# Kernel tuning notes

Hardware: AMD Instinct MI355X
Metric: run time of the kernel (lower is better)

Reference implementation:

```python
import jax, jax.numpy as jnp
import numpy as np

EMBED, HEADS, LEVELS, POINTS, FFN = 256, 8, 4, 4, 1024
HD = EMBED // HEADS


def layer_norm(x, g, b, eps=1e-5):
    m = jnp.mean(x, axis=-1, keepdims=True)
    v = jnp.mean((x - m) ** 2, axis=-1, keepdims=True)
    return (x - m) / jnp.sqrt(v + eps) * g + b


def ms_deform_attn_core(value, shapes_np, loc, attn):
    # value: (B, nk, H, hd); loc: (B, nq, H, L, P, 2) normalized [0,1]; attn: (B, nq, H, L, P)
    B, nq = loc.shape[0], loc.shape[1]
    splits = np.cumsum(shapes_np[:, 0] * shapes_np[:, 1])[:-1]
    vals = jnp.split(value, splits, axis=1)
    out = jnp.zeros((B, HEADS, nq, HD), value.dtype)
    for l in range(LEVELS):
        Hl, Wl = int(shapes_np[l, 0]), int(shapes_np[l, 1])
        v = vals[l].transpose(0, 2, 1, 3)                     # (B, H, Hl*Wl, hd)
        x = loc[:, :, :, l, :, 0] * Wl - 0.5                  # (B, nq, H, P) pixel coords
        y = loc[:, :, :, l, :, 1] * Hl - 0.5
        x0 = jnp.floor(x); y0 = jnp.floor(y)
        fx = x - x0; fy = y - y0
        x0i = x0.astype(jnp.int32); y0i = y0.astype(jnp.int32)
        acc = jnp.zeros((B, HEADS, nq * POINTS, HD), value.dtype)
        for dx, dy, w in ((0, 0, (1 - fx) * (1 - fy)), (1, 0, fx * (1 - fy)),
                          (0, 1, (1 - fx) * fy), (1, 1, fx * fy)):
            xi = x0i + dx; yi = y0i + dy
            valid = (xi >= 0) & (xi < Wl) & (yi >= 0) & (yi < Hl)
            idx = jnp.clip(yi, 0, Hl - 1) * Wl + jnp.clip(xi, 0, Wl - 1)  # (B, nq, H, P)
            idx_f = idx.transpose(0, 2, 1, 3).reshape(B, HEADS, -1)
            g = jnp.take_along_axis(v, idx_f[..., None], axis=2)          # (B, H, nq*P, hd)
            wv = jnp.where(valid, w, 0.0).transpose(0, 2, 1, 3).reshape(B, HEADS, -1, 1)
            acc = acc + g * wv
        aw = attn[:, :, :, l].transpose(0, 2, 1, 3).reshape(B, HEADS, -1, 1)
        out = out + (acc * aw).reshape(B, HEADS, nq, POINTS, HD).sum(3)
    return out.transpose(0, 2, 1, 3).reshape(B, nq, EMBED)


def setup_inputs() -> dict:
    key = jax.random.key(0)
    ks = jax.random.split(key, 20)
    B = 2
    shapes = np.array([[136, 136], [68, 68], [34, 34], [17, 17]], np.int32)
    nk = int((shapes[:, 0] * shapes[:, 1]).sum())  # 24565
    lsi = np.concatenate([[0], np.cumsum(shapes[:, 0] * shapes[:, 1])[:-1]]).astype(np.int32)

    def lin(k, i, o):
        return jax.random.normal(k, (i, o), jnp.float32) * 0.02

    return {
        "src": jax.random.normal(ks[0], (B, nk, EMBED), jnp.float32),
        "reference_points": jax.random.uniform(ks[1], (B, nk, LEVELS, 2), jnp.float32),
        "spatial_shapes": jnp.asarray(shapes),
        "level_start_index": jnp.asarray(lsi),
        "w_off": lin(ks[2], EMBED, HEADS * LEVELS * POINTS * 2),
        "b_off": jax.random.normal(ks[3], (HEADS * LEVELS * POINTS * 2,), jnp.float32) * 0.5,
        "w_att": lin(ks[4], EMBED, HEADS * LEVELS * POINTS),
        "b_att": jnp.zeros((HEADS * LEVELS * POINTS,), jnp.float32),
        "w_val": lin(ks[5], EMBED, EMBED), "b_val": jnp.zeros((EMBED,), jnp.float32),
        "w_out": lin(ks[6], EMBED, EMBED), "b_out": jnp.zeros((EMBED,), jnp.float32),
        "g1": jnp.ones((EMBED,), jnp.float32), "bt1": jnp.zeros((EMBED,), jnp.float32),
        "w1": lin(ks[7], EMBED, FFN), "b1": jnp.zeros((FFN,), jnp.float32),
        "w2": lin(ks[8], FFN, EMBED), "b2": jnp.zeros((EMBED,), jnp.float32),
        "g2": jnp.ones((EMBED,), jnp.float32), "bt2": jnp.zeros((EMBED,), jnp.float32),
    }


def reference(src, reference_points, spatial_shapes, level_start_index,
              w_off, b_off, w_att, b_att, w_val, b_val, w_out, b_out,
              g1, bt1, w1, b1, w2, b2, g2, bt2):
    B, nq, D = src.shape
    shapes_np = np.asarray(spatial_shapes)
    # projections
    value = (src @ w_val + b_val).reshape(B, nq, HEADS, HD)
    off = (src @ w_off + b_off).reshape(B, nq, HEADS, LEVELS, POINTS, 2)
    attn = (src @ w_att + b_att).reshape(B, nq, HEADS, LEVELS * POINTS)
    attn = jax.nn.softmax(attn, axis=-1).reshape(B, nq, HEADS, LEVELS, POINTS)
    # sampling locations: ref + offset / [W, H] per level
    normalizer = jnp.asarray(shapes_np[:, ::-1].copy(), src.dtype)  # (L, 2) = [W, H]
    loc = reference_points[:, :, None, :, None, :] + off / normalizer[None, None, None, :, None, :]
    attn_out = ms_deform_attn_core(value, shapes_np, loc, attn) @ w_out + b_out
    x = layer_norm(src + attn_out, g1, bt1)
    ffn = jax.nn.relu(x @ w1 + b1) @ w2 + b2
    return layer_norm(x + ffn, g2, bt2)
```

## Files before the change

### kernel.cpp

```cpp
#include <hip/hip_runtime.h>
#include <math.h>

#define EMBED 256
#define HEADS 8
#define LEVELS 4
#define POINTS 4
#define FFNDIM 1024

typedef float f32x4 __attribute__((ext_vector_type(4)));
typedef float f32x2 __attribute__((ext_vector_type(2)));
typedef __bf16 bf16x8 __attribute__((ext_vector_type(8)));

static __device__ __forceinline__ float4 ld4f(const float* p) {
    return *reinterpret_cast<const float4*>(p);
}
static __device__ __forceinline__ unsigned short f2bf(float f) {
    unsigned int u = __float_as_uint(f);
    unsigned int r = (u + 0x7fffu + ((u >> 16) & 1u)) >> 16;
    return (unsigned short)r;
}
static __device__ __forceinline__ float bf2f(unsigned short u) {
    return __uint_as_float((unsigned int)u << 16);
}
static __device__ __forceinline__ f32x2 pkfma(f32x2 a, f32x2 b, f32x2 c) {
#if __has_builtin(__builtin_elementwise_fma)
    return __builtin_elementwise_fma(a, b, c);
#else
    f32x2 r; r.x = fmaf(a.x, b.x, c.x); r.y = fmaf(a.y, b.y, c.y); return r;
#endif
}
static __device__ __forceinline__
void gl_lds16(const unsigned short* g, unsigned short* l) {
    __builtin_amdgcn_global_load_lds(
        (const __attribute__((address_space(1))) unsigned int*)g,
        (__attribute__((address_space(3))) unsigned int*)l, 16, 0, 0);
}

__global__ __launch_bounds__(256)
void k_cvt_src(const float* __restrict__ src, unsigned short* __restrict__ dst, int n)
{
    int i = (blockIdx.x * 256 + threadIdx.x) * 4;
    const int stride = gridDim.x * 1024;
    for (; i < n; i += stride) {
        float4 v = ld4f(src + i);
        ushort4 o;
        o.x = f2bf(v.x); o.y = f2bf(v.y); o.z = f2bf(v.z); o.w = f2bf(v.w);
        *reinterpret_cast<ushort4*>(dst + i) = o;
    }
}

__global__ __launch_bounds__(256)
void k_cvt_w(const float* __restrict__ wv, const float* __restrict__ wo,
             const float* __restrict__ wa, const float* __restrict__ wout,
             const float* __restrict__ w1, const float* __restrict__ w2,
             unsigned short* __restrict__ wcat, unsigned short* __restrict__ woutt,
             unsigned short* __restrict__ w1t, unsigned short* __restrict__ w2t)
{
    const int total = 163840 + 65536 + 262144 + 262144;
    for (int gid = blockIdx.x * 256 + threadIdx.x; gid < total; gid += gridDim.x * 256) {
        int local = gid;
        float f; unsigned short* dst;
        if (local < 163840) {
            int n = local >> 8, k = local & 255;
            if (n < 256)      f = wv[k * 256 + n];
            else if (n < 512) f = wo[k * 256 + (n - 256)];
            else              f = wa[k * 128 + (n - 512)];
            dst = wcat + local;
        } else if ((local -= 163840) < 65536) {
            int n = local >> 8, k = local & 255;
            f = wout[k * 256 + n];
            dst = woutt + local;
        } else if ((local -= 65536) < 262144) {
            int n = local >> 8, k = local & 255;
            f = w1[k * 1024 + n];
            dst = w1t + local;
        } else {
            local -= 262144;
            int n = local >> 10, k = local & 1023;
            f = w2[k * 256 + n];
            dst = w2t + local;
        }
        *dst = f2bf(f);
    }
}


#define GEMM_STAGE(Aptr, ASTR, Wptr, WSTR, kcexp)                              \
    {                                                                          \
        int row = (wid << 3) + (lane >> 3);                                    \
        int slot = (lane & 7) ^ (row & 7);                                     \
        gl_lds16(Aptr + (size_t)(m0 + row) * ASTR + (kcexp) * 64 + slot * 8,   \
                 a_s + (size_t)(wid << 3) * 64);                               \
    }                                                                          \
    _Pragma("unroll")                                                          \
    for (int rnd = 0; rnd < 4; ++rnd) {                                        \
        int row = (rnd << 6) + (wid << 3) + (lane >> 3);                       \
        int slot = (lane & 7) ^ (row & 7);                                     \
        gl_lds16(Wptr + (size_t)(n0 + row) * WSTR + (kcexp) * 64 + slot * 8,   \
                 w_s + (size_t)((rnd << 6) + (wid << 3)) * 64);                \
    }

#define GEMM_FRAGS_MFMA                                                        \
    {                                                                          \
        bf16x8 af[2][2], bfr[4][2];                                            \
        const int ksb = (lane >> 4);                                           \
        _Pragma("unroll")                                                      \
        for (int i = 0; i < 2; ++i) {                                          \
            int m = wm * 32 + i * 16 + cl;                                     \
            _Pragma("unroll")                                                  \
            for (int kk = 0; kk < 2; ++kk) {                                   \
                int phys = (kk * 4 + ksb) ^ (m & 7);                           \
                af[i][kk] = *reinterpret_cast<const bf16x8*>(                  \
                    a_s + m * 64 + phys * 8);                                  \
            }                                                                  \
        }                                                                      \
        _Pragma("unroll")                                                      \
        for (int j = 0; j < 4; ++j) {                                          \
            int n = wn * 64 + j * 16 + cl;                                     \
            _Pragma("unroll")                                                  \
            for (int kk = 0; kk < 2; ++kk) {                                   \
                int phys = (kk * 4 + ksb) ^ (n & 7);                           \
                bfr[j][kk] = *reinterpret_cast<const bf16x8*>(                 \
                    w_s + n * 64 + phys * 8);                                  \
            }                                                                  \
        }                                                                      \
        _Pragma("unroll")                                                      \
        for (int kk = 0; kk < 2; ++kk)                                         \
            _Pragma("unroll")                                                  \
            for (int i = 0; i < 2; ++i)                                        \
                _Pragma("unroll")                                              \
                for (int j = 0; j < 4; ++j)                                    \
                    acc[i][j] = __builtin_amdgcn_mfma_f32_16x16x32_bf16(       \
                        af[i][kk], bfr[j][kk], acc[i][j], 0, 0, 0);            \
    }

__global__ __launch_bounds__(512)
void k_proj(const unsigned short* __restrict__ A, const unsigned short* __restrict__ Wt,
            const float* __restrict__ b_val, const float* __restrict__ b_off,
            const float* __restrict__ b_att,
            unsigned short* __restrict__ value, unsigned short* __restrict__ offr,
            unsigned short* __restrict__ attw, int M, int nk)
{
    __shared__ __align__(16) unsigned short smem[20480];
    unsigned short* a_s = smem;
    unsigned short* w_s = smem + 4096;
    const int tid = threadIdx.x;
    const int m0 = blockIdx.x * 64;
    const int y = blockIdx.y;
    const int n0 = y * 256;
    const int lane = tid & 63, wid = tid >> 6;
    const int wm = wid >> 2, wn = wid & 3;
    const int cl = lane & 15, r4 = (lane >> 4) * 4;

    f32x4 acc[2][4] = {};

    for (int kc = 0; kc < 4; ++kc) {
        __syncthreads();
        GEMM_STAGE(A, 256, Wt, 256, kc)
        __syncthreads();
        GEMM_FRAGS_MFMA
    }

    if (y < 2) {
        const float* bias = (y == 0) ? b_val : b_off;
        __syncthreads();
        #pragma unroll
        for (int j = 0; j < 4; ++j) {
            int col = wn * 64 + j * 16 + cl;
            float bv = bias[col];
            #pragma unroll
            for (int i = 0; i < 2; ++i)
                #pragma unroll
                for (int r = 0; r < 4; ++r)
                    smem[(wm * 32 + i * 16 + r4 + r) * 264 + col] = f2bf(acc[i][j][r] + bv);
        }
        __syncthreads();
        if (y == 0) {
            #pragma unroll
            for (int t = 0; t < 4; ++t) {
                int idx = tid + t * 512;
                int row = idx >> 5, cu = idx & 31;
                int grow = m0 + row;
                if (grow < M) {
                    int b = grow >= nk;
                    int pix = grow - (b ? nk : 0);
                    int hh = cu >> 2, ch = (cu & 3) * 8;
                    *reinterpret_cast<uint4*>(
                        value + ((size_t)(b * 8 + hh) * nk + pix) * 32 + ch) =
                        *reinterpret_cast<const uint4*>(smem + row * 264 + cu * 8);
                }
            }
        } else {
            #pragma unroll
            for (int t = 0; t < 4; ++t) {
                int idx = tid + t * 512;
                int row = idx >> 5, cu = idx & 31;
                int grow = m0 + row;
                if (grow < M)
                    *reinterpret_cast<uint4*>(offr + (size_t)grow * 256 + cu * 8) =
                        *reinterpret_cast<const uint4*>(smem + row * 264 + cu * 8);
            }
        }
    } else {
        if (wn < 2) {
            #pragma unroll
            for (int j = 0; j < 4; ++j) {
                int a = wn * 64 + j * 16 + cl;
                float bv = b_att[a];
                #pragma unroll
                for (int i = 0; i < 2; ++i) {
                    #pragma unroll
                    for (int r = 0; r < 4; ++r) {
                        float v = acc[i][j][r] + bv;
                        float mx = v;
                        mx = fmaxf(mx, __shfl_xor(mx, 1));
                        mx = fmaxf(mx, __shfl_xor(mx, 2));
                        mx = fmaxf(mx, __shfl_xor(mx, 4));
                        mx = fmaxf(mx, __shfl_xor(mx, 8));
                        float e = __expf(v - mx);
                        float s = e;
                        s += __shfl_xor(s, 1);
                        s += __shfl_xor(s, 2);
                        s += __shfl_xor(s, 4);
                        s += __shfl_xor(s, 8);
                        acc[i][j][r] = e / s;
                    }
                }
            }
        }
        __syncthreads();
        if (wn < 2) {
            #pragma unroll
            for (int j = 0; j < 4; ++j) {
                int a = wn * 64 + j * 16 + cl;
                #pragma unroll
                for (int i = 0; i < 2; ++i)
                    #pragma unroll
                    for (int r = 0; r < 4; ++r)
                        smem[(wm * 32 + i * 16 + r4 + r) * 136 + a] = f2bf(acc[i][j][r]);
            }
        }
        __syncthreads();
        #pragma unroll
        for (int t = 0; t < 2; ++t) {
            int idx = tid + t * 512;
            int row = idx >> 4, cu = idx & 15;
            int grow = m0 + row;
            if (grow < M)
                *reinterpret_cast<uint4*>(attw + (size_t)grow * 128 + cu * 8) =
                    *reinterpret_cast<const uint4*>(smem + row * 136 + cu * 8);
        }
    }
}

__global__ __launch_bounds__(256)
void k_sample(const unsigned short* __restrict__ value,
              const unsigned short* __restrict__ offr,
              const unsigned short* __restrict__ attw,
              const float* __restrict__ ref,
              const int* __restrict__ shapes, const int* __restrict__ lsi,
              unsigned short* __restrict__ core, int M)
{
    __shared__ int2 iw_s[64][65];
    const int tid = threadIdx.x;
    const int bh = blockIdx.x & 15;
    const int grp = blockIdx.x >> 4;
    const int b = bh >> 3, h = bh & 7;
    const int nk = lsi[3] + shapes[6] * shapes[7];
    const int tok0 = grp * 64;

    #pragma unroll
    for (int rnd = 0; rnd < 4; ++rnd) {
        const int lp = tid & 15;
        const int tk = rnd * 16 + (tid >> 4);
        const int l = lp >> 2;
        const int pix0 = tok0 + tk;
        int2 out[4];
        if (pix0 < nk) {
            const int token = b * nk + pix0;
            const int Hl = shapes[l * 2], Wl = shapes[l * 2 + 1];
            const int pbase = bh * nk + lsi[l];
            const float rx = ref[(size_t)token * 8 + l * 2];
            const float ry = ref[(size_t)token * 8 + l * 2 + 1];
            const unsigned int oxy = *reinterpret_cast<const unsigned int*>(
                offr + (size_t)token * 256 + (h * 16 + lp) * 2);
            const float ox = bf2f((unsigned short)(oxy & 0xffffu));
            const float oy = bf2f((unsigned short)(oxy >> 16));
            const float aw = bf2f(attw[(size_t)token * 128 + h * 16 + lp]);
            const float x = fmaf(rx, (float)Wl, ox) - 0.5f;
            const float y = fmaf(ry, (float)Hl, oy) - 0.5f;
            const float x0f = floorf(x), y0f = floorf(y);
            const float fx = x - x0f, fy = y - y0f;
            const int x0 = (int)x0f, y0 = (int)y0f;
            #pragma unroll
            for (int t = 0; t < 4; ++t) {
                const int dx = t & 1, dy = t >> 1;
                const int xi = x0 + dx, yi = y0 + dy;
                const bool valid = (xi >= 0) & (xi < Wl) & (yi >= 0) & (yi < Hl);
                const float w = (dx ? fx : 1.f - fx) * (dy ? fy : 1.f - fy) * aw;
                const int xc = min(max(xi, 0), Wl - 1);
                const int yc = min(max(yi, 0), Hl - 1);
                out[t].x = (pbase + yc * Wl + xc) * 16;
                out[t].y = __float_as_int(valid ? w : 0.f);
            }
        } else {
            #pragma unroll
            for (int t = 0; t < 4; ++t) out[t] = make_int2(0, 0);
        }
        #pragma unroll
        for (int t = 0; t < 4; ++t)
            iw_s[lp * 4 + t][tk] = out[t];
    }
    __syncthreads();

    const int tk = tid >> 2;
    const int dp = tid & 3;
    const int pix = tok0 + tk;
    const unsigned int* vu = reinterpret_cast<const unsigned int*>(value) + dp * 4;
    f32x2 a0 = {0.f, 0.f}, a1 = {0.f, 0.f};
    f32x2 a2 = {0.f, 0.f}, a3 = {0.f, 0.f};
    #pragma unroll 16
    for (int q = 0; q < 64; ++q) {
        const int2 iw = iw_s[q][tk];
        const float w = __int_as_float(iw.y);
        const f32x2 w2 = {w, w};
        const uint4 v = *reinterpret_cast<const uint4*>(vu + (size_t)(unsigned)iw.x);
        const f32x2 v0 = {__uint_as_float(v.x << 16), __uint_as_float(v.x & 0xffff0000u)};
        const f32x2 v1 = {__uint_as_float(v.y << 16), __uint_as_float(v.y & 0xffff0000u)};
        const f32x2 v2 = {__uint_as_float(v.z << 16), __uint_as_float(v.z & 0xffff0000u)};
        const f32x2 v3 = {__uint_as_float(v.w << 16), __uint_as_float(v.w & 0xffff0000u)};
        a0 = pkfma(v0, w2, a0);
        a1 = pkfma(v1, w2, a1);
        a2 = pkfma(v2, w2, a2);
        a3 = pkfma(v3, w2, a3);
    }
    if (pix < nk) {
        uint4 o;
        o.x = (unsigned int)f2bf(a0.x) | ((unsigned int)f2bf(a0.y) << 16);
        o.y = (unsigned int)f2bf(a1.x) | ((unsigned int)f2bf(a1.y) << 16);
        o.z = (unsigned int)f2bf(a2.x) | ((unsigned int)f2bf(a2.y) << 16);
        o.w = (unsigned int)f2bf(a3.x) | ((unsigned int)f2bf(a3.y) << 16);
        *reinterpret_cast<uint4*>(
            core + (size_t)(b * nk + pix) * 256 + h * 32 + dp * 8) = o;
    }
}

__global__ __launch_bounds__(512)
void k_oproj(const unsigned short* __restrict__ A, const unsigned short* __restrict__ Wt,
             const float* __restrict__ b_out, const float* __restrict__ src,
             const float* __restrict__ g1, const float* __restrict__ bt1,
             unsigned short* __restrict__ X, int M)
{
    __shared__ __align__(16) unsigned short smem[20480];
    unsigned short* a_s = smem;
    unsigned short* w_s = smem + 4096;
    __shared__ float red[64 * 8];
    __shared__ float mr[64 * 2];
    const int tid = threadIdx.x;
    const int m0 = blockIdx.x * 64;
    const int n0 = 0;
    const int lane = tid & 63, wid = tid >> 6;
    const int wm = wid >> 2, wn = wid & 3;
    const int cl = lane & 15, r4 = (lane >> 4) * 4;

    f32x4 acc[2][4] = {};

    for (int kc = 0; kc < 4; ++kc) {
        __syncthreads();
        GEMM_STAGE(A, 256, Wt, 256, kc)
        __syncthreads();
        GEMM_FRAGS_MFMA
    }

    #pragma unroll
    for (int j = 0; j < 4; ++j) {
        int col = wn * 64 + j * 16 + cl;
        float bv = b_out[col];
        #pragma unroll
        for (int i = 0; i < 2; ++i) {
            int mb = wm * 32 + i * 16 + r4;
            #pragma unroll
            for (int r = 0; r < 4; ++r) {
                int row = m0 + mb + r;
                float sv = (row < M) ? src[(size_t)row * 256 + col] : 0.f;
                acc[i][j][r] += bv + sv;
            }
        }
    }
    #pragma unroll
    for (int i = 0; i < 2; ++i)
        #pragma unroll
        for (int r = 0; r < 4; ++r) {
            float s1 = 0.f, s2 = 0.f;
            #pragma unroll
            for (int j = 0; j < 4; ++j) { float t = acc[i][j][r]; s1 += t; s2 += t * t; }
            s1 += __shfl_xor(s1, 1); s2 += __shfl_xor(s2, 1);
            s1 += __shfl_xor(s1, 2); s2 += __shfl_xor(s2, 2);
            s1 += __shfl_xor(s1, 4); s2 += __shfl_xor(s2, 4);
            s1 += __shfl_xor(s1, 8); s2 += __shfl_xor(s2, 8);
            if (cl == 0) {
                int rr = wm * 32 + i * 16 + r4 + r;
                red[(rr * 4 + wn) * 2 + 0] = s1;
                red[(rr * 4 + wn) * 2 + 1] = s2;
            }
        }
    __syncthreads();
    if (tid < 64) {
        float s1 = red[tid * 8] + red[tid * 8 + 2] + red[tid * 8 + 4] + red[tid * 8 + 6];
        float s2 = red[tid * 8 + 1] + red[tid * 8 + 3] + red[tid * 8 + 5] + red[tid * 8 + 7];
        float mu = s1 * (1.f / 256.f);
        mr[tid * 2] = mu;
        mr[tid * 2 + 1] = rsqrtf(fmaxf(s2 * (1.f / 256.f) - mu * mu, 0.f) + 1e-5f);
    }
    __syncthreads();
    #pragma unroll
    for (int j = 0; j < 4; ++j) {
        int col = wn * 64 + j * 16 + cl;
        float gv = g1[col], bt = bt1[col];
        #pragma unroll
        for (int i = 0; i < 2; ++i)
            #pragma unroll
            for (int r = 0; r < 4; ++r) {
                int rr = wm * 32 + i * 16 + r4 + r;
                smem[rr * 264 + col] =
                    f2bf((acc[i][j][r] - mr[rr * 2]) * mr[rr * 2 + 1] * gv + bt);
            }
    }
    __syncthreads();
    #pragma unroll
    for (int t = 0; t < 4; ++t) {
        int idx = tid + t * 512;
        int row = idx >> 5, cu = idx & 31;
        int grow = m0 + row;
        if (grow < M)
            *reinterpret_cast<uint4*>(X + (size_t)grow * 256 + cu * 8) =
                *reinterpret_cast<const uint4*>(smem + row * 264 + cu * 8);
    }
}

__global__ __launch_bounds__(512)
void k_ffn1(const unsigned short* __restrict__ A, const unsigned short* __restrict__ W1t,
            const float* __restrict__ B1, unsigned short* __restrict__ h, int M)
{
    __shared__ __align__(16) unsigned short smem[20480];
    unsigned short* a_s = smem;
    unsigned short* w_s = smem + 4096;
    const int tid = threadIdx.x;
    const int m0 = blockIdx.x * 64;
    const int n0 = blockIdx.y * 256;
    const int lane = tid & 63, wid = tid >> 6;
    const int wm = wid >> 2, wn = wid & 3;
    const int cl = lane & 15, r4 = (lane >> 4) * 4;

    f32x4 acc[2][4] = {};

    for (int kc = 0; kc < 4; ++kc) {
        __syncthreads();
        GEMM_STAGE(A, 256, W1t, 256, kc)
        __syncthreads();
        GEMM_FRAGS_MFMA
    }

    __syncthreads();
    #pragma unroll
    for (int j = 0; j < 4; ++j) {
        int col = wn * 64 + j * 16 + cl;
        float bv = B1[n0 + col];
        #pragma unroll
        for (int i = 0; i < 2; ++i)
            #pragma unroll
            for (int r = 0; r < 4; ++r)
                smem[(wm * 32 + i * 16 + r4 + r) * 264 + col] =
                    f2bf(fmaxf(acc[i][j][r] + bv, 0.f));
    }
    __syncthreads();
    #pragma unroll
    for (int t = 0; t < 4; ++t) {
        int idx = tid + t * 512;
        int row = idx >> 5, cu = idx & 31;
        int grow = m0 + row;
        if (grow < M)
            *reinterpret_cast<uint4*>(h + (size_t)grow * 1024 + n0 + cu * 8) =
                *reinterpret_cast<const uint4*>(smem + row * 264 + cu * 8);
    }
}

__global__ __launch_bounds__(512)
void k_ffn2(const unsigned short* __restrict__ h, const unsigned short* __restrict__ W2t,
            const float* __restrict__ B2, const unsigned short* __restrict__ Xbf,
            const float* __restrict__ G2, const float* __restrict__ BT2,
            float* __restrict__ OUT, int M)
{
    __shared__ __align__(16) unsigned short smem[20480];
    unsigned short* a_s = smem;
    unsigned short* w_s = smem + 4096;
    __shared__ float red[64 * 8];
    __shared__ float mr[64 * 2];
    const int tid = threadIdx.x;
    const int m0 = blockIdx.x * 64;
    const int n0 = 0;
    const int lane = tid & 63, wid = tid >> 6;
    const int wm = wid >> 2, wn = wid & 3;
    const int cl = lane & 15, r4 = (lane >> 4) * 4;

    f32x4 acc[2][4] = {};

    for (int kc = 0; kc < 16; ++kc) {
        __syncthreads();
        GEMM_STAGE(h, 1024, W2t, 1024, kc)
        __syncthreads();
        GEMM_FRAGS_MFMA
    }

    #pragma unroll
    for (int j = 0; j < 4; ++j) {
        int col = wn * 64 + j * 16 + cl;
        float bv = B2[col];
        #pragma unroll
        for (int i = 0; i < 2; ++i) {
            int mb = wm * 32 + i * 16 + r4;
            #pragma unroll
            for (int r = 0; r < 4; ++r) {
                int row = m0 + mb + r;
                float xv = (row < M) ? bf2f(Xbf[(size_t)row * 256 + col]) : 0.f;
                acc[i][j][r] += bv + xv;
            }
        }
    }
    #pragma unroll
    for (int i = 0; i < 2; ++i)
        #pragma unroll
        for (int r = 0; r < 4; ++r) {
            float s1 = 0.f, s2 = 0.f;
            #pragma unroll
            for (int j = 0; j < 4; ++j) { float t = acc[i][j][r]; s1 += t; s2 += t * t; }
            s1 += __shfl_xor(s1, 1); s2 += __shfl_xor(s2, 1);
            s1 += __shfl_xor(s1, 2); s2 += __shfl_xor(s2, 2);
            s1 += __shfl_xor(s1, 4); s2 += __shfl_xor(s2, 4);
            s1 += __shfl_xor(s1, 8); s2 += __shfl_xor(s2, 8);
            if (cl == 0) {
                int rr = wm * 32 + i * 16 + r4 + r;
                red[(rr * 4 + wn) * 2 + 0] = s1;
                red[(rr * 4 + wn) * 2 + 1] = s2;
            }
        }
    __syncthreads();
    if (tid < 64) {
        float s1 = red[tid * 8] + red[tid * 8 + 2] + red[tid * 8 + 4] + red[tid * 8 + 6];
        float s2 = red[tid * 8 + 1] + red[tid * 8 + 3] + red[tid * 8 + 5] + red[tid * 8 + 7];
        float mu = s1 * (1.f / 256.f);
        mr[tid * 2] = mu;
        mr[tid * 2 + 1] = rsqrtf(fmaxf(s2 * (1.f / 256.f) - mu * mu, 0.f) + 1e-5f);
    }
    __syncthreads();
    #pragma unroll
    for (int j = 0; j < 4; ++j) {
        int col = wn * 64 + j * 16 + cl;
        float gv = G2[col], bt = BT2[col];
        #pragma unroll
        for (int i = 0; i < 2; ++i) {
            int mb = wm * 32 + i * 16 + r4;
            #pragma unroll
            for (int r = 0; r < 4; ++r) {
                int rr = mb + r, row = m0 + rr;
                if (row < M)
                    OUT[(size_t)row * 256 + col] =
                        (acc[i][j][r] - mr[rr * 2]) * mr[rr * 2 + 1] * gv + bt;
            }
        }
    }
}

extern "C" void kernel_launch(void* const* d_in, const int* in_sizes, int n_in,
                              void* d_out, int out_size, void* d_ws, size_t ws_size,
                              hipStream_t stream) {
    const float* src    = (const float*)d_in[0];
    const float* ref    = (const float*)d_in[1];
    const int*   shapes = (const int*)d_in[2];
    const int*   lsi    = (const int*)d_in[3];
    const float* b_off  = (const float*)d_in[5];
    const float* b_att  = (const float*)d_in[7];
    const float* b_val  = (const float*)d_in[9];
    const float* b_out  = (const float*)d_in[11];
    const float* g1     = (const float*)d_in[12];
    const float* bt1    = (const float*)d_in[13];
    const float* b1     = (const float*)d_in[15];
    const float* b2     = (const float*)d_in[17];
    const float* g2     = (const float*)d_in[18];
    const float* bt2    = (const float*)d_in[19];
    const float* w_off  = (const float*)d_in[4];
    const float* w_att  = (const float*)d_in[6];
    const float* w_val  = (const float*)d_in[8];
    const float* w_out  = (const float*)d_in[10];
    const float* w1     = (const float*)d_in[14];
    const float* w2     = (const float*)d_in[16];

    const int M = in_sizes[0] / EMBED;
    const int nk = M / 2;
    const size_t M256 = (size_t)M * 256;

    unsigned short* w16     = (unsigned short*)d_ws;
    unsigned short* src_bf  = w16;
    unsigned short* value_bf = src_bf + M256;
    unsigned short* offr_bf = value_bf + M256;
    unsigned short* core_bf = offr_bf + M256;
    unsigned short* x_bf    = core_bf + M256;
    unsigned short* attw_bf = x_bf + M256;
    unsigned short* wcat    = attw_bf + (size_t)M * 128;
    unsigned short* woutt   = wcat + 163840;
    unsigned short* w1t     = woutt + 65536;
    unsigned short* w2t     = w1t + 262144;
    unsigned short* h_bf    = w16;

    const int gb64 = (M + 63) / 64;
    const int ngrp = (nk + 63) / 64;

    k_cvt_src<<<4096, 256, 0, stream>>>(src, src_bf, M * 256);
    k_cvt_w<<<2944, 256, 0, stream>>>(w_val, w_off, w_att, w_out, w1, w2,
                                      wcat, woutt, w1t, w2t);
    k_proj<<<dim3(gb64, 3), 512, 0, stream>>>(src_bf, wcat, b_val, b_off, b_att,
                                              value_bf, offr_bf, attw_bf, M, nk);
    k_sample<<<ngrp * 16, 256, 0, stream>>>(value_bf, offr_bf, attw_bf, ref,
                                            shapes, lsi, core_bf, M);
    k_oproj<<<gb64, 512, 0, stream>>>(core_bf, woutt, b_out, src, g1, bt1, x_bf, M);
    k_ffn1<<<dim3(gb64, 4), 512, 0, stream>>>(x_bf, w1t, b1, h_bf, M);
    k_ffn2<<<gb64, 512, 0, stream>>>(h_bf, w2t, b2, x_bf, g2, bt2,
                                     (float*)d_out, M);
}
```

Baseline: 258.8 us.

## Keep full-K A tile resident in LDS and loop over N slabs per block

The projection, output-projection and FFN1 GEMMs now stage the whole 64x256 activation tile into LDS once, then iterate over the N slabs (value/offset/attention, or the four FFN1 column slabs) inside one block instead of launching a grid dimension per slab. This avoids re-reading the A tile from global memory for every N slab. The epilogue is split into two half-row passes so it fits in the weight buffer. In exchange, LDS per block grows to 64 KB, which can cut occupancy, and the grid shrinks by 3-4x, so the GPU is filled with fewer, longer blocks.

```diff
diff --git a/kernel.cpp b/kernel.cpp
--- a/kernel.cpp
+++ b/kernel.cpp
@@ -85,33 +85,37 @@
 }
 
 
-#define GEMM_STAGE(Aptr, ASTR, Wptr, WSTR, kcexp)                              \
-    {                                                                          \
-        int row = (wid << 3) + (lane >> 3);                                    \
-        int slot = (lane & 7) ^ (row & 7);                                     \
-        gl_lds16(Aptr + (size_t)(m0 + row) * ASTR + (kcexp) * 64 + slot * 8,   \
-                 a_s + (size_t)(wid << 3) * 64);                               \
-    }                                                                          \
+#define STAGE_A_RES(Aptr, ASTR)                                                \
     _Pragma("unroll")                                                          \
-    for (int rnd = 0; rnd < 4; ++rnd) {                                        \
+    for (int it = 0; it < 4; ++it) {                                           \
+        int g = it * 512 + wid * 64 + lane;                                    \
+        int row = g >> 5, c = g & 31;                                          \
+        int s = c ^ (row & 7);                                                 \
+        gl_lds16(Aptr + (size_t)(m0 + row) * ASTR + s * 8,                     \
+                 a_s + (size_t)(it * 512 + wid * 64) * 8);                     \
+    }
+
+#define STAGE_W_SLAB(Wptr, WSTR, NRND, kcexp)                                  \
+    _Pragma("unroll")                                                          \
+    for (int rnd = 0; rnd < NRND; ++rnd) {                                     \
         int row = (rnd << 6) + (wid << 3) + (lane >> 3);                       \
         int slot = (lane & 7) ^ (row & 7);                                     \
         gl_lds16(Wptr + (size_t)(n0 + row) * WSTR + (kcexp) * 64 + slot * 8,   \
                  w_s + (size_t)((rnd << 6) + (wid << 3)) * 64);                \
     }
 
-#define GEMM_FRAGS_MFMA                                                        \
+#define KSTEP_4J(kcv)                                                          \
     {                                                                          \
+        const int ksb = (lane >> 4);                                           \
         bf16x8 af[2][2], bfr[4][2];                                            \
-        const int ksb = (lane >> 4);                                           \
         _Pragma("unroll")                                                      \
         for (int i = 0; i < 2; ++i) {                                          \
             int m = wm * 32 + i * 16 + cl;                                     \
             _Pragma("unroll")                                                  \
             for (int kk = 0; kk < 2; ++kk) {                                   \
-                int phys = (kk * 4 + ksb) ^ (m & 7);                           \
+                int phys = (kcv) * 8 + (((kk << 2) + ksb) ^ (m & 7));          \
                 af[i][kk] = *reinterpret_cast<const bf16x8*>(                  \
-                    a_s + m * 64 + phys * 8);                                  \
+                    a_s + m * 256 + phys * 8);                                 \
             }                                                                  \
         }                                                                      \
         _Pragma("unroll")                                                      \
@@ -119,7 +123,7 @@
             int n = wn * 64 + j * 16 + cl;                                     \
             _Pragma("unroll")                                                  \
             for (int kk = 0; kk < 2; ++kk) {                                   \
-                int phys = (kk * 4 + ksb) ^ (n & 7);                           \
+                int phys = ((kk << 2) + ksb) ^ (n & 7);                        \
                 bfr[j][kk] = *reinterpret_cast<const bf16x8*>(                 \
                     w_s + n * 64 + phys * 8);                                  \
             }                                                                  \
@@ -141,104 +145,137 @@
             unsigned short* __restrict__ value, unsigned short* __restrict__ offr,
             unsigned short* __restrict__ attw, int M, int nk)
 {
-    __shared__ __align__(16) unsigned short smem[20480];
-    unsigned short* a_s = smem;
-    unsigned short* w_s = smem + 4096;
+    __shared__ __align__(16) unsigned short a_s[64 * 256];
+    __shared__ __align__(16) unsigned short w_s[256 * 64];
     const int tid = threadIdx.x;
     const int m0 = blockIdx.x * 64;
-    const int y = blockIdx.y;
-    const int n0 = y * 256;
     const int lane = tid & 63, wid = tid >> 6;
     const int wm = wid >> 2, wn = wid & 3;
     const int cl = lane & 15, r4 = (lane >> 4) * 4;
 
-    f32x4 acc[2][4] = {};
-
-    for (int kc = 0; kc < 4; ++kc) {
-        __syncthreads();
-        GEMM_STAGE(A, 256, Wt, 256, kc)
-        __syncthreads();
-        GEMM_FRAGS_MFMA
-    }
-
-    if (y < 2) {
-        const float* bias = (y == 0) ? b_val : b_off;
-        __syncthreads();
-        #pragma unroll
-        for (int j = 0; j < 4; ++j) {
-            int col = wn * 64 + j * 16 + cl;
-            float bv = bias[col];
-            #pragma unroll
-            for (int i = 0; i < 2; ++i)
-                #pragma unroll
-                for (int r = 0; r < 4; ++r)
-                    smem[(wm * 32 + i * 16 + r4 + r) * 264 + col] = f2bf(acc[i][j][r] + bv);
-        }
-        __syncthreads();
-        if (y == 0) {
-            #pragma unroll
-            for (int t = 0; t < 4; ++t) {
+    STAGE_A_RES(A, 256)
+
+    for (int sl = 0; sl < 2; ++sl) {
+        const int n0 = sl * 256;
+        f32x4 acc[2][4] = {};
+        for (int kc = 0; kc < 4; ++kc) {
+            __syncthreads();
+            STAGE_W_SLAB(Wt, 256, 4, kc)
+            __syncthreads();
+            KSTEP_4J(kc)
+        }
+        const float* bias = (sl == 0) ? b_val : b_off;
+        #pragma unroll
+        for (int hh = 0; hh < 2; ++hh) {
+            __syncthreads();
+            if (wm == hh) {
+                #pragma unroll
+                for (int j = 0; j < 4; ++j) {
+                    int col = wn * 64 + j * 16 + cl;
+                    float bv = bias[col];
+                    #pragma unroll
+                    for (int i = 0; i < 2; ++i)
+                        #pragma unroll
+                        for (int r = 0; r < 4; ++r)
+                            w_s[(i * 16 + r4 + r) * 264 + col] =
+                                f2bf(acc[i][j][r] + bv);
+                }
+            }
+            __syncthreads();
+            #pragma unroll
+            for (int t = 0; t < 2; ++t) {
                 int idx = tid + t * 512;
                 int row = idx >> 5, cu = idx & 31;
-                int grow = m0 + row;
+                int grow = m0 + hh * 32 + row;
                 if (grow < M) {
-                    int b = grow >= nk;
-                    int pix = grow - (b ? nk : 0);
-                    int hh = cu >> 2, ch = (cu & 3) * 8;
-                    *reinterpret_cast<uint4*>(
-                        value + ((size_t)(b * 8 + hh) * nk + pix) * 32 + ch) =
-                        *reinterpret_cast<const uint4*>(smem + row * 264 + cu * 8);
-                }
-            }
-        } else {
-            #pragma unroll
-            for (int t = 0; t < 4; ++t) {
-                int idx = tid + t * 512;
-                int row = idx >> 5, cu = idx & 31;
-                int grow = m0 + row;
-                if (grow < M)
-                    *reinterpret_cast<uint4*>(offr + (size_t)grow * 256 + cu * 8) =
-                        *reinterpret_cast<const uint4*>(smem + row * 264 + cu * 8);
-            }
-        }
-    } else {
-        if (wn < 2) {
-            #pragma unroll
-            for (int j = 0; j < 4; ++j) {
-                int a = wn * 64 + j * 16 + cl;
-                float bv = b_att[a];
-                #pragma unroll
-                for (int i = 0; i < 2; ++i) {
-                    #pragma unroll
-                    for (int r = 0; r < 4; ++r) {
-                        float v = acc[i][j][r] + bv;
-                        float mx = v;
-                        mx = fmaxf(mx, __shfl_xor(mx, 1));
-                        mx = fmaxf(mx, __shfl_xor(mx, 2));
-                        mx = fmaxf(mx, __shfl_xor(mx, 4));
-                        mx = fmaxf(mx, __shfl_xor(mx, 8));
-                        float e = __expf(v - mx);
-                        float s = e;
-                        s += __shfl_xor(s, 1);
-                        s += __shfl_xor(s, 2);
-                        s += __shfl_xor(s, 4);
-                        s += __shfl_xor(s, 8);
-                        acc[i][j][r] = e / s;
+                    uint4 vv = *reinterpret_cast<const uint4*>(w_s + row * 264 + cu * 8);
+                    if (sl == 0) {
+                        int b = grow >= nk;
+                        int pix = grow - (b ? nk : 0);
+                        int hd = cu >> 2, ch = (cu & 3) * 8;
+                        *reinterpret_cast<uint4*>(
+                            value + ((size_t)(b * 8 + hd) * nk + pix) * 32 + ch) = vv;
+                    } else {
+                        *reinterpret_cast<uint4*>(offr + (size_t)grow * 256 + cu * 8) = vv;
                     }
                 }
             }
         }
+    }
+
+    {
+        const int n0 = 512;
+        f32x4 acc[2][2] = {};
+        for (int kc = 0; kc < 4; ++kc) {
+            __syncthreads();
+            STAGE_W_SLAB(Wt, 256, 2, kc)
+            __syncthreads();
+            {
+                const int ksb = (lane >> 4);
+                bf16x8 af[2][2], bfr[2][2];
+                #pragma unroll
+                for (int i = 0; i < 2; ++i) {
+                    int m = wm * 32 + i * 16 + cl;
+                    #pragma unroll
+                    for (int kk = 0; kk < 2; ++kk) {
+                        int phys = kc * 8 + (((kk << 2) + ksb) ^ (m & 7));
+                        af[i][kk] = *reinterpret_cast<const bf16x8*>(
+                            a_s + m * 256 + phys * 8);
+                    }
+                }
+                #pragma unroll
+                for (int j = 0; j < 2; ++j) {
+                    int n = wn * 32 + j * 16 + cl;
+                    #pragma unroll
+                    for (int kk = 0; kk < 2; ++kk) {
+                        int phys = ((kk << 2) + ksb) ^ (n & 7);
+                        bfr[j][kk] = *reinterpret_cast<const bf16x8*>(
+                            w_s + n * 64 + phys * 8);
+                    }
+                }
+                #pragma unroll
+                for (int kk = 0; kk < 2; ++kk)
+                    #pragma unroll
+                    for (int i = 0; i < 2; ++i)
+                        #pragma unroll
+                        for (int j = 0; j < 2; ++j)
+                            acc[i][j] = __builtin_amdgcn_mfma_f32_16x16x32_bf16(
+                                af[i][kk], bfr[j][kk], acc[i][j], 0, 0, 0);
+            }
+        }
+        #pragma unroll
+        for (int j = 0; j < 2; ++j) {
+            int a = wn * 32 + j * 16 + cl;
+            float bv = b_att[a];
+            #pragma unroll
+            for (int i = 0; i < 2; ++i) {
+                #pragma unroll
+                for (int r = 0; r < 4; ++r) {
+                    float v = acc[i][j][r] + bv;
+                    float mx = v;
+                    mx = fmaxf(mx, __shfl_xor(mx, 1));
+                    mx = fmaxf(mx, __shfl_xor(mx, 2));
+                    mx = fmaxf(mx, __shfl_xor(mx, 4));
+                    mx = fmaxf(mx, __shfl_xor(mx, 8));
+                    float e = __expf(v - mx);
+                    float s = e;
+                    s += __shfl_xor(s, 1);
+                    s += __shfl_xor(s, 2);
+                    s += __shfl_xor(s, 4);
+                    s += __shfl_xor(s, 8);
+                    acc[i][j][r] = e / s;
+                }
+            }
+        }
         __syncthreads();
-        if (wn < 2) {
-            #pragma unroll
-            for (int j = 0; j < 4; ++j) {
-                int a = wn * 64 + j * 16 + cl;
-                #pragma unroll
-                for (int i = 0; i < 2; ++i)
-                    #pragma unroll
-                    for (int r = 0; r < 4; ++r)
-                        smem[(wm * 32 + i * 16 + r4 + r) * 136 + a] = f2bf(acc[i][j][r]);
-            }
+        #pragma unroll
+        for (int j = 0; j < 2; ++j) {
+            int a = wn * 32 + j * 16 + cl;
+            #pragma unroll
+            for (int i = 0; i < 2; ++i)
+                #pragma unroll
+                for (int r = 0; r < 4; ++r)
+                    w_s[(wm * 32 + i * 16 + r4 + r) * 136 + a] = f2bf(acc[i][j][r]);
         }
         __syncthreads();
         #pragma unroll
@@ -248,7 +285,7 @@
             int grow = m0 + row;
             if (grow < M)
                 *reinterpret_cast<uint4*>(attw + (size_t)grow * 128 + cu * 8) =
-                    *reinterpret_cast<const uint4*>(smem + row * 136 + cu * 8);
+                    *reinterpret_cast<const uint4*>(w_s + row * 136 + cu * 8);
         }
     }
 }
@@ -351,9 +388,8 @@
              const float* __restrict__ g1, const float* __restrict__ bt1,
              unsigned short* __restrict__ X, int M)
 {
-    __shared__ __align__(16) unsigned short smem[20480];
-    unsigned short* a_s = smem;
-    unsigned short* w_s = smem + 4096;
+    __shared__ __align__(16) unsigned short a_s[64 * 256];
+    __shared__ __align__(16) unsigned short w_s[256 * 64];
     __shared__ float red[64 * 8];
     __shared__ float mr[64 * 2];
     const int tid = threadIdx.x;
@@ -363,13 +399,14 @@
     const int wm = wid >> 2, wn = wid & 3;
     const int cl = lane & 15, r4 = (lane >> 4) * 4;
 
+    STAGE_A_RES(A, 256)
+
     f32x4 acc[2][4] = {};
-
     for (int kc = 0; kc < 4; ++kc) {
         __syncthreads();
-        GEMM_STAGE(A, 256, Wt, 256, kc)
+        STAGE_W_SLAB(Wt, 256, 4, kc)
         __syncthreads();
-        GEMM_FRAGS_MFMA
+        KSTEP_4J(kc)
     }
 
     #pragma unroll
@@ -414,27 +451,34 @@
     }
     __syncthreads();
     #pragma unroll
-    for (int j = 0; j < 4; ++j) {
-        int col = wn * 64 + j * 16 + cl;
-        float gv = g1[col], bt = bt1[col];
-        #pragma unroll
-        for (int i = 0; i < 2; ++i)
-            #pragma unroll
-            for (int r = 0; r < 4; ++r) {
-                int rr = wm * 32 + i * 16 + r4 + r;
-                smem[rr * 264 + col] =
-                    f2bf((acc[i][j][r] - mr[rr * 2]) * mr[rr * 2 + 1] * gv + bt);
-            }
-    }
-    __syncthreads();
-    #pragma unroll
-    for (int t = 0; t < 4; ++t) {
-        int idx = tid + t * 512;
-        int row = idx >> 5, cu = idx & 31;
-        int grow = m0 + row;
-        if (grow < M)
-            *reinterpret_cast<uint4*>(X + (size_t)grow * 256 + cu * 8) =
-                *reinterpret_cast<const uint4*>(smem + row * 264 + cu * 8);
+    for (int hh = 0; hh < 2; ++hh) {
+        __syncthreads();
+        if (wm == hh) {
+            #pragma unroll
+            for (int j = 0; j < 4; ++j) {
+                int col = wn * 64 + j * 16 + cl;
+                float gv = g1[col], bt = bt1[col];
+                #pragma unroll
+                for (int i = 0; i < 2; ++i)
+                    #pragma unroll
+                    for (int r = 0; r < 4; ++r) {
+                        int lr = i * 16 + r4 + r;
+                        int rr = hh * 32 + lr;
+                        w_s[lr * 264 + col] =
+                            f2bf((acc[i][j][r] - mr[rr * 2]) * mr[rr * 2 + 1] * gv + bt);
+                    }
+            }
+        }
+        __syncthreads();
+        #pragma unroll
+        for (int t = 0; t < 2; ++t) {
+            int idx = tid + t * 512;
+            int row = idx >> 5, cu = idx & 31;
+            int grow = m0 + hh * 32 + row;
+            if (grow < M)
+                *reinterpret_cast<uint4*>(X + (size_t)grow * 256 + cu * 8) =
+                    *reinterpret_cast<const uint4*>(w_s + row * 264 + cu * 8);
+        }
     }
 }
 
@@ -442,48 +486,69 @@
 void k_ffn1(const unsigned short* __restrict__ A, const unsigned short* __restrict__ W1t,
             const float* __restrict__ B1, unsigned short* __restrict__ h, int M)
 {
-    __shared__ __align__(16) unsigned short smem[20480];
-    unsigned short* a_s = smem;
-    unsigned short* w_s = smem + 4096;
+    __shared__ __align__(16) unsigned short a_s[64 * 256];
+    __shared__ __align__(16) unsigned short w_s[256 * 64];
     const int tid = threadIdx.x;
     const int m0 = blockIdx.x * 64;
-    const int n0 = blockIdx.y * 256;
     const int lane = tid & 63, wid = tid >> 6;
     const int wm = wid >> 2, wn = wid & 3;
     const int cl = lane & 15, r4 = (lane >> 4) * 4;
 
-    f32x4 acc[2][4] = {};
-
-    for (int kc = 0; kc < 4; ++kc) {
-        __syncthreads();
-        GEMM_STAGE(A, 256, W1t, 256, kc)
-        __syncthreads();
-        GEMM_FRAGS_MFMA
-    }
-
-    __syncthreads();
-    #pragma unroll
-    for (int j = 0; j < 4; ++j) {
-        int col = wn * 64 + j * 16 + cl;
-        float bv = B1[n0 + col];
-        #pragma unroll
-        for (int i = 0; i < 2; ++i)
-            #pragma unroll
-            for (int r = 0; r < 4; ++r)
-                smem[(wm * 32 + i * 16 + r4 + r) * 264 + col] =
-                    f2bf(fmaxf(acc[i][j][r] + bv, 0.f));
-    }
-    __syncthreads();
-    #pragma unroll
-    for (int t = 0; t < 4; ++t) {
-        int idx = tid + t * 512;
-        int row = idx >> 5, cu = idx & 31;
-        int grow = m0 + row;
-        if (grow < M)
-            *reinterpret_cast<uint4*>(h + (size_t)grow * 1024 + n0 + cu * 8) =
-                *reinterpret_cast<const uint4*>(smem + row * 264 + cu * 8);
-    }
-}
+    STAGE_A_RES(A, 256)
+
+    for (int sl = 0; sl < 4; ++sl) {
+        const int n0 = sl * 256;
+        f32x4 acc[2][4] = {};
+        for (int kc = 0; kc < 4; ++kc) {
+            __syncthreads();
+            STAGE_W_SLAB(W1t, 256, 4, kc)
+            __syncthreads();
+            KSTEP_4J(kc)
+        }
+        #pragma unroll
+        for (int hh = 0; hh < 2; ++hh) {
+            __syncthreads();
+            if (wm == hh) {
+                #pragma unroll
+                for (int j = 0; j < 4; ++j) {
+                    int col = wn * 64 + j * 16 + cl;
+                    float bv = B1[n0 + col];
+                    #pragma unroll
+                    for (int i = 0; i < 2; ++i)
+                        #pragma unroll
+                        for (int r = 0; r < 4; ++r)
+                            w_s[(i * 16 + r4 + r) * 264 + col] =
+                                f2bf(fmaxf(acc[i][j][r] + bv, 0.f));
+                }
+            }
+            __syncthreads();
+            #pragma unroll
+            for (int t = 0; t < 2; ++t) {
+                int idx = tid + t * 512;
+                int row = idx >> 5, cu = idx & 31;
+                int grow = m0 + hh * 32 + row;
+                if (grow < M)
+                    *reinterpret_cast<uint4*>(h + (size_t)grow * 1024 + n0 + cu * 8) =
+                        *reinterpret_cast<const uint4*>(w_s + row * 264 + cu * 8);
+            }
+        }
+    }
+}
+
+#define GEMM_STAGE2(Aptr, ASTR, Wptr, WSTR, kcexp)                             \
+    {                                                                          \
+        int row = (wid << 3) + (lane >> 3);                                    \
+        int slot = (lane & 7) ^ (row & 7);                                     \
+        gl_lds16(Aptr + (size_t)(m0 + row) * ASTR + (kcexp) * 64 + slot * 8,   \
+                 a2_s + (size_t)(wid << 3) * 64);                              \
+    }                                                                          \
+    _Pragma("unroll")                                                          \
+    for (int rnd = 0; rnd < 4; ++rnd) {                                        \
+        int row = (rnd << 6) + (wid << 3) + (lane >> 3);                       \
+        int slot = (lane & 7) ^ (row & 7);                                     \
+        gl_lds16(Wptr + (size_t)row * WSTR + (kcexp) * 64 + slot * 8,          \
+                 w2_s + (size_t)((rnd << 6) + (wid << 3)) * 64);               \
+    }
 
 __global__ __launch_bounds__(512)
 void k_ffn2(const unsigned short* __restrict__ h, const unsigned short* __restrict__ W2t,
@@ -492,13 +557,12 @@
             float* __restrict__ OUT, int M)
 {
     __shared__ __align__(16) unsigned short smem[20480];
-    unsigned short* a_s = smem;
-    unsigned short* w_s = smem + 4096;
+    unsigned short* a2_s = smem;
+    unsigned short* w2_s = smem + 4096;
     __shared__ float red[64 * 8];
     __shared__ float mr[64 * 2];
     const int tid = threadIdx.x;
     const int m0 = blockIdx.x * 64;
-    const int n0 = 0;
     const int lane = tid & 63, wid = tid >> 6;
     const int wm = wid >> 2, wn = wid & 3;
     const int cl = lane & 15, r4 = (lane >> 4) * 4;
@@ -507,9 +571,40 @@
 
     for (int kc = 0; kc < 16; ++kc) {
         __syncthreads();
-        GEMM_STAGE(h, 1024, W2t, 1024, kc)
+        GEMM_STAGE2(h, 1024, W2t, 1024, kc)
         __syncthreads();
-        GEMM_FRAGS_MFMA
+        {
+            const int ksb = (lane >> 4);
+            bf16x8 af[2][2], bfr[4][2];
+            #pragma unroll
+            for (int i = 0; i < 2; ++i) {
+                int m = wm * 32 + i * 16 + cl;
+                #pragma unroll
+                for (int kk = 0; kk < 2; ++kk) {
+                    int phys = ((kk << 2) + ksb) ^ (m & 7);
+                    af[i][kk] = *reinterpret_cast<const bf16x8*>(
+                        a2_s + m * 64 + phys * 8);
+                }
+            }
+            #pragma unroll
+            for (int j = 0; j < 4; ++j) {
+                int n = wn * 64 + j * 16 + cl;
+                #pragma unroll
+                for (int kk = 0; kk < 2; ++kk) {
+                    int phys = ((kk << 2) + ksb) ^ (n & 7);
+                    bfr[j][kk] = *reinterpret_cast<const bf16x8*>(
+                        w2_s + n * 64 + phys * 8);
+                }
+            }
+            #pragma unroll
+            for (int kk = 0; kk < 2; ++kk)
+                #pragma unroll
+                for (int i = 0; i < 2; ++i)
+                    #pragma unroll
+                    for (int j = 0; j < 4; ++j)
+                        acc[i][j] = __builtin_amdgcn_mfma_f32_16x16x32_bf16(
+                            af[i][kk], bfr[j][kk], acc[i][j], 0, 0, 0);
+        }
     }
 
     #pragma unroll
@@ -618,12 +713,12 @@
     k_cvt_src<<<4096, 256, 0, stream>>>(src, src_bf, M * 256);
     k_cvt_w<<<2944, 256, 0, stream>>>(w_val, w_off, w_att, w_out, w1, w2,
                                       wcat, woutt, w1t, w2t);
-    k_proj<<<dim3(gb64, 3), 512, 0, stream>>>(src_bf, wcat, b_val, b_off, b_att,
-                                              value_bf, offr_bf, attw_bf, M, nk);
+    k_proj<<<gb64, 512, 0, stream>>>(src_bf, wcat, b_val, b_off, b_att,
+                                     value_bf, offr_bf, attw_bf, M, nk);
     k_sample<<<ngrp * 16, 256, 0, stream>>>(value_bf, offr_bf, attw_bf, ref,
                                             shapes, lsi, core_bf, M);
     k_oproj<<<gb64, 512, 0, stream>>>(core_bf, woutt, b_out, src, g1, bt1, x_bf, M);
-    k_ffn1<<<dim3(gb64, 4), 512, 0, stream>>>(x_bf, w1t, b1, h_bf, M);
+    k_ffn1<<<gb64, 512, 0, stream>>>(x_bf, w1t, b1, h_bf, M);
     k_ffn2<<<gb64, 512, 0, stream>>>(h_bf, w2t, b2, x_bf, g2, bt2,
                                      (float*)d_out, M);
 }
```

New measurement: 279.7 us. 1.08x slower.
